# Performance work log

Hardware: AMD Instinct MI355X
Metric: run time of the kernel (lower is better)

The kernel has to match this reference:

```python
import jax, jax.numpy as jnp
import numpy as np

B, L, DIM, H = 2, 2048, 1024, 16
HD = DIM // H  # head dim = 64
MASK_SCALE = -10 * 6  # faithful to the original source: mask_expand *= -10 * 6


def setup_inputs() -> dict:
    key = jax.random.key(0)
    ks = jax.random.split(key, 8)
    s = 1.0 / np.sqrt(DIM)
    return {
        "x": jax.random.normal(ks[0], (B, L, DIM), jnp.float32),
        "attention_mask": jax.random.uniform(ks[1], (B, L, L), jnp.float32),
        "Wq": jax.random.normal(ks[2], (DIM, DIM), jnp.float32) * s,
        "bq": jnp.zeros((DIM,), jnp.float32),
        "Wk": jax.random.normal(ks[3], (DIM, DIM), jnp.float32) * s,
        "bk": jnp.zeros((DIM,), jnp.float32),
        "Wv": jax.random.normal(ks[4], (DIM, DIM), jnp.float32) * s,
        "bv": jnp.zeros((DIM,), jnp.float32),
    }


def _split_heads(t):
    # [B, L, DIM] -> [B, H, L, HD]
    return t.reshape(B, L, H, HD).transpose(0, 2, 1, 3)


def reference(x, attention_mask, Wq, bq, Wk, bk, Wv, bv):
    q = _split_heads(x @ Wq + bq)
    k = _split_heads(x @ Wk + bk)
    v = _split_heads(x @ Wv + bv)
    scale = float(HD) ** -0.5
    # full [B, H, L, L] score matrix, as in the original
    scores = jnp.einsum("bhqd,bhkd->bhqk", q, k) * scale
    scores = scores + attention_mask[:, None, :, :] * MASK_SCALE
    probs = jax.nn.softmax(scores, axis=-1)
    ctx = jnp.einsum("bhqk,bhkd->bhqd", probs, v)
    # merge heads back: [B, L, DIM]
    return ctx.transpose(0, 2, 1, 3).reshape(B, L, DIM)
```

## Files before the change

### kernel.cpp

```cpp
#include <hip/hip_runtime.h>

#define LL 2048
#define NHEADS 16
#define HDIM 64
#define QSCALE 0.18033688011112042f
#define MASKC1 -86.56170245333780f

typedef __attribute__((ext_vector_type(8))) __bf16 bf16x8;
typedef __attribute__((ext_vector_type(4))) float f32x4;

__device__ __forceinline__ unsigned short f2bf(float f) {
  unsigned int u = __builtin_bit_cast(unsigned int, f);
  u += 0x7fffu + ((u >> 16) & 1u);
  return (unsigned short)(u >> 16);
}

__device__ __forceinline__ bf16x8 ld_frag(const unsigned short* p) {
  return *reinterpret_cast<const bf16x8*>(p);
}

__device__ __forceinline__ void async_cp16(const unsigned short* g, unsigned short* l) {
  __builtin_amdgcn_global_load_lds(
      (const __attribute__((address_space(1))) unsigned int*)(unsigned long long)(g),
      (__attribute__((address_space(3))) unsigned int*)(unsigned int)(unsigned long long)(l),
      16, 0, 0);
}

__global__ __launch_bounds__(256) void cvt_x_kernel(const float* __restrict__ x,
                                                    unsigned short* __restrict__ xb) {
  int i = (blockIdx.x * 256 + threadIdx.x) * 4;
  float4 v = *reinterpret_cast<const float4*>(x + i);
  ushort4 o;
  o.x = f2bf(v.x); o.y = f2bf(v.y); o.z = f2bf(v.z); o.w = f2bf(v.w);
  *reinterpret_cast<ushort4*>(xb + i) = o;
}

__global__ __launch_bounds__(256) void transpose_w_kernel(const float* __restrict__ Wq,
                                                          const float* __restrict__ Wk,
                                                          const float* __restrict__ Wv,
                                                          unsigned short* __restrict__ WtAll) {
  int z = blockIdx.z;
  const float* W = (z == 0) ? Wq : (z == 1) ? Wk : Wv;
  unsigned short* dst = WtAll + (size_t)z * 1024 * 1024;
  int n0 = blockIdx.x * 64, k0 = blockIdx.y * 64;
  __shared__ float t[64][65];
  int tx = threadIdx.x & 63, ty = threadIdx.x >> 6;
#pragma unroll
  for (int p = 0; p < 16; ++p) {
    int kr = p * 4 + ty;
    t[kr][tx] = W[(size_t)(k0 + kr) * 1024 + n0 + tx];
  }
  __syncthreads();
#pragma unroll
  for (int p = 0; p < 16; ++p) {
    int nr = p * 4 + ty;
    dst[(size_t)(n0 + nr) * 1024 + k0 + tx] = f2bf(t[tx][nr]);
  }
}

__global__ __launch_bounds__(256) void em_prep_kernel(const float* __restrict__ mask,
                                                      unsigned short* __restrict__ em) {
  int row = blockIdx.y;
  int t = blockIdx.x * 256 + threadIdx.x;
  int kb = t >> 4, c = t & 15;
  const float* src = mask + (size_t)row * LL + kb * 64 + c;
  ushort4 o;
  o.x = f2bf(__builtin_amdgcn_exp2f(src[0]  * MASKC1));
  o.y = f2bf(__builtin_amdgcn_exp2f(src[16] * MASKC1));
  o.z = f2bf(__builtin_amdgcn_exp2f(src[32] * MASKC1));
  o.w = f2bf(__builtin_amdgcn_exp2f(src[48] * MASKC1));
  *reinterpret_cast<ushort4*>(em + (size_t)row * LL + kb * 64 + 4 * c) = o;
}

__global__ __launch_bounds__(256) void qkv_gemm_kernel(
    const unsigned short* __restrict__ xb, const unsigned short* __restrict__ WtAll,
    const float* __restrict__ bq, const float* __restrict__ bk, const float* __restrict__ bv,
    unsigned short* __restrict__ qkv) {
  const int z = blockIdx.z;
  const unsigned short* Wt = WtAll + (size_t)z * 1024 * 1024;
  const float* bias = (z == 0) ? bq : (z == 1) ? bk : bv;
  unsigned short* outb = qkv + (size_t)z * 4194304;

  __shared__ __align__(16) unsigned short smem[16384];
  unsigned short* As = smem;
  unsigned short* Bs = smem + 8192;

  const int tid = threadIdx.x;
  const int w = tid >> 6, lane = tid & 63, g = lane >> 4, cc = lane & 15;
  const int wm = w >> 1, wn = w & 1;
  const int m0 = blockIdx.y * 128, n0 = blockIdx.x * 128;
  const int srow = lane >> 3;
  const int gc = ((lane & 7) - srow) & 7;
  const unsigned short* ga = xb + (size_t)(m0 + w * 32 + srow) * 1024 + gc * 8;
  const unsigned short* gb = Wt + (size_t)(n0 + w * 32 + srow) * 1024 + gc * 8;
  unsigned short* la = As + w * 2048;
  unsigned short* lb = Bs + w * 2048;

  f32x4 acc[4][4];
#pragma unroll
  for (int i = 0; i < 4; ++i)
#pragma unroll
    for (int j = 0; j < 4; ++j) acc[i][j] = (f32x4)0.0f;

  for (int kk = 0; kk < 1024; kk += 64) {
    __syncthreads();
#pragma unroll
    for (int i = 0; i < 4; ++i) {
      async_cp16(ga + i * 8192 + kk, la + i * 512);
      async_cp16(gb + i * 8192 + kk, lb + i * 512);
    }
    __syncthreads();
    bf16x8 af[4][2], bfr[4][2];
#pragma unroll
    for (int mt = 0; mt < 4; ++mt)
#pragma unroll
      for (int ks = 0; ks < 2; ++ks)
        af[mt][ks] = ld_frag(&As[(wm * 64 + mt * 16 + cc) * 64 + ((4 * ks + g + cc) & 7) * 8]);
#pragma unroll
    for (int nt = 0; nt < 4; ++nt)
#pragma unroll
      for (int ks = 0; ks < 2; ++ks)
        bfr[nt][ks] = ld_frag(&Bs[(wn * 64 + nt * 16 + cc) * 64 + ((4 * ks + g + cc) & 7) * 8]);
#pragma unroll
    for (int mt = 0; mt < 4; ++mt)
#pragma unroll
      for (int nt = 0; nt < 4; ++nt)
#pragma unroll
        for (int ks = 0; ks < 2; ++ks)
          acc[mt][nt] = __builtin_amdgcn_mfma_f32_16x16x32_bf16(af[mt][ks], bfr[nt][ks],
                                                                acc[mt][nt], 0, 0, 0);
  }

  if (z != 2) {
    const float sc = (z == 0) ? QSCALE : 1.0f;
#pragma unroll
    for (int nt = 0; nt < 4; ++nt) {
      int n = n0 + wn * 64 + nt * 16 + cc;
      float bval = bias[n];
      int h = n >> 6, d = n & 63;
#pragma unroll
      for (int mt = 0; mt < 4; ++mt) {
#pragma unroll
        for (int r = 0; r < 4; ++r) {
          int m = m0 + wm * 64 + mt * 16 + g * 4 + r;
          int b = m >> 11, l = m & 2047;
          outb[(((size_t)(b * NHEADS + h) * LL) + l) * HDIM + d] =
              f2bf((acc[mt][nt][r] + bval) * sc);
        }
      }
    }
  } else {
    __syncthreads();
#pragma unroll
    for (int nt = 0; nt < 4; ++nt) {
      int nr = wn * 64 + nt * 16 + cc;
      float bval = bias[n0 + nr];
#pragma unroll
      for (int mt = 0; mt < 4; ++mt)
#pragma unroll
        for (int r = 0; r < 4; ++r)
          smem[nr * 128 + wm * 64 + 16 * g + 4 * r + mt] = f2bf(acc[mt][nt][r] + bval);
    }
    __syncthreads();
    int row = tid >> 1, half = tid & 1;
    int n = n0 + row, hh = n >> 6, dd = n & 63;
    int bb = m0 >> 11, l0 = (m0 & 2047) + half * 64;
    unsigned short* dst = outb + ((size_t)(bb * NHEADS + hh) * HDIM + dd) * LL + l0;
#pragma unroll
    for (int i = 0; i < 8; ++i)
      *reinterpret_cast<uint4*>(dst + i * 8) =
          *reinterpret_cast<const uint4*>(&smem[row * 128 + half * 64 + i * 8]);
  }
}

__global__ __launch_bounds__(256) void flash_kernel(
    const unsigned short* __restrict__ Qb, const unsigned short* __restrict__ Kb,
    const unsigned short* __restrict__ Vt, const unsigned short* __restrict__ Em,
    float* __restrict__ out) {
  const int bh = blockIdx.y, b = bh >> 4, h = bh & 15;
  const int q0 = blockIdx.x * 128;
  const int tid = threadIdx.x, w = tid >> 6, lane = tid & 63, g = lane >> 4, cc = lane & 15;
  const size_t bhoff = (size_t)bh * LL * HDIM;

  __shared__ __align__(16) unsigned short Ps[128 * 72];
  __shared__ __align__(16) unsigned short Ks[2][64 * 64];
  __shared__ __align__(16) unsigned short Vs[2][64 * 64];

  bf16x8 aq[2][2];
#pragma unroll
  for (int mt = 0; mt < 2; ++mt)
#pragma unroll
    for (int ks = 0; ks < 2; ++ks)
      aq[mt][ks] = *reinterpret_cast<const bf16x8*>(
          Qb + bhoff + (size_t)(q0 + w * 32 + mt * 16 + cc) * HDIM + ks * 32 + g * 8);

  const int srow = lane >> 3;
  const int gcs = ((lane & 7) - srow) & 7;
  const unsigned short* kg0 = Kb + bhoff + (size_t)(w * 8 + srow) * HDIM + gcs * 8;
  const unsigned short* kg1 = Kb + bhoff + (size_t)(32 + w * 8 + srow) * HDIM + gcs * 8;
  const unsigned short* vg0 = Vt + bhoff + (size_t)(w * 8 + srow) * LL + gcs * 8;
  const unsigned short* vg1 = Vt + bhoff + (size_t)(32 + w * 8 + srow) * LL + gcs * 8;

  float li[2][4];
  f32x4 oacc[2][4];
#pragma unroll
  for (int mt = 0; mt < 2; ++mt) {
#pragma unroll
    for (int r = 0; r < 4; ++r) li[mt][r] = 0.0f;
#pragma unroll
    for (int nt = 0; nt < 4; ++nt) oacc[mt][nt] = (f32x4)0.0f;
  }

  const unsigned short* embase = Em + ((size_t)b * LL + q0 + w * 32) * LL + 4 * cc;

  {
    async_cp16(kg0, Ks[0] + w * 512);
    async_cp16(kg1, Ks[0] + (w + 4) * 512);
    async_cp16(vg0, Vs[0] + w * 512);
    async_cp16(vg1, Vs[0] + (w + 4) * 512);
  }

  for (int kt = 0; kt < 32; ++kt) {
    const int buf = kt & 1;
    __syncthreads();
    if (kt + 1 < 32) {
      const int nb = buf ^ 1;
      async_cp16(kg0 + (size_t)(kt + 1) * 64 * HDIM, Ks[nb] + w * 512);
      async_cp16(kg1 + (size_t)(kt + 1) * 64 * HDIM, Ks[nb] + (w + 4) * 512);
      async_cp16(vg0 + (kt + 1) * 64, Vs[nb] + w * 512);
      async_cp16(vg1 + (kt + 1) * 64, Vs[nb] + (w + 4) * 512);
    }
    uint2 emv[2][4];
#pragma unroll
    for (int mt = 0; mt < 2; ++mt)
#pragma unroll
      for (int r = 0; r < 4; ++r)
        emv[mt][r] = *reinterpret_cast<const uint2*>(
            embase + (size_t)(mt * 16 + g * 4 + r) * LL + kt * 64);

    bf16x8 bk_[4][2];
#pragma unroll
    for (int nt = 0; nt < 4; ++nt)
#pragma unroll
      for (int ks = 0; ks < 2; ++ks)
        bk_[nt][ks] =
            ld_frag(&Ks[buf][(nt * 16 + cc) * 64 + ((4 * ks + g + cc) & 7) * 8]);
    f32x4 sacc[2][4];
#pragma unroll
    for (int mt = 0; mt < 2; ++mt)
#pragma unroll
      for (int nt = 0; nt < 4; ++nt) sacc[mt][nt] = (f32x4)0.0f;
#pragma unroll
    for (int mt = 0; mt < 2; ++mt)
#pragma unroll
      for (int nt = 0; nt < 4; ++nt)
#pragma unroll
        for (int ks = 0; ks < 2; ++ks)
          sacc[mt][nt] = __builtin_amdgcn_mfma_f32_16x16x32_bf16(aq[mt][ks], bk_[nt][ks],
                                                                 sacc[mt][nt], 0, 0, 0);

#pragma unroll
    for (int mt = 0; mt < 2; ++mt) {
#pragma unroll
      for (int r = 0; r < 4; ++r) {
        unsigned int ex = emv[mt][r].x, ey = emv[mt][r].y;
        float e0 = __builtin_bit_cast(float, ex << 16);
        float e1 = __builtin_bit_cast(float, ex & 0xffff0000u);
        float e2 = __builtin_bit_cast(float, ey << 16);
        float e3 = __builtin_bit_cast(float, ey & 0xffff0000u);
        float p0 = __builtin_amdgcn_exp2f(sacc[mt][0][r]) * e0;
        float p1 = __builtin_amdgcn_exp2f(sacc[mt][1][r]) * e1;
        float p2 = __builtin_amdgcn_exp2f(sacc[mt][2][r]) * e2;
        float p3 = __builtin_amdgcn_exp2f(sacc[mt][3][r]) * e3;
        unsigned int u01 = __builtin_amdgcn_perm(__builtin_bit_cast(unsigned int, p1),
                                                 __builtin_bit_cast(unsigned int, p0),
                                                 0x07060302u);
        unsigned int u23 = __builtin_amdgcn_perm(__builtin_bit_cast(unsigned int, p3),
                                                 __builtin_bit_cast(unsigned int, p2),
                                                 0x07060302u);
        li[mt][r] += __builtin_bit_cast(float, u01 << 16) +
                     __builtin_bit_cast(float, u01 & 0xffff0000u) +
                     __builtin_bit_cast(float, u23 << 16) +
                     __builtin_bit_cast(float, u23 & 0xffff0000u);
        uint2 pk; pk.x = u01; pk.y = u23;
        *reinterpret_cast<uint2*>(&Ps[(w * 32 + mt * 16 + g * 4 + r) * 72 + 4 * cc]) = pk;
      }
    }
    asm volatile("" ::: "memory");

    bf16x8 ap[2][2], bv[4][2];
#pragma unroll
    for (int mt = 0; mt < 2; ++mt)
#pragma unroll
      for (int ks = 0; ks < 2; ++ks)
        ap[mt][ks] = ld_frag(&Ps[(w * 32 + mt * 16 + cc) * 72 + ks * 32 + g * 8]);
#pragma unroll
    for (int nt = 0; nt < 4; ++nt)
#pragma unroll
      for (int ks = 0; ks < 2; ++ks)
        bv[nt][ks] =
            ld_frag(&Vs[buf][(nt * 16 + cc) * 64 + ((4 * ks + g + cc) & 7) * 8]);
#pragma unroll
    for (int mt = 0; mt < 2; ++mt)
#pragma unroll
      for (int nt = 0; nt < 4; ++nt)
#pragma unroll
        for (int ks = 0; ks < 2; ++ks)
          oacc[mt][nt] = __builtin_amdgcn_mfma_f32_16x16x32_bf16(ap[mt][ks], bv[nt][ks],
                                                                 oacc[mt][nt], 0, 0, 0);
  }

#pragma unroll
  for (int mt = 0; mt < 2; ++mt)
#pragma unroll
    for (int r = 0; r < 4; ++r) {
      float s = li[mt][r];
      s += __shfl_xor(s, 1);
      s += __shfl_xor(s, 2);
      s += __shfl_xor(s, 4);
      s += __shfl_xor(s, 8);
      float inv = 1.0f / s;
      int qrow = q0 + w * 32 + mt * 16 + g * 4 + r;
#pragma unroll
      for (int nt = 0; nt < 4; ++nt)
        out[((size_t)b * LL + qrow) * 1024 + h * 64 + nt * 16 + cc] = oacc[mt][nt][r] * inv;
    }
}

extern "C" void kernel_launch(void* const* d_in, const int* in_sizes, int n_in,
                              void* d_out, int out_size, void* d_ws, size_t ws_size,
                              hipStream_t stream) {
  const float* x    = (const float*)d_in[0];
  const float* mask = (const float*)d_in[1];
  const float* Wq   = (const float*)d_in[2];
  const float* bq   = (const float*)d_in[3];
  const float* Wk   = (const float*)d_in[4];
  const float* bk   = (const float*)d_in[5];
  const float* Wv   = (const float*)d_in[6];
  const float* bv   = (const float*)d_in[7];
  float* out = (float*)d_out;
  (void)in_sizes; (void)n_in; (void)out_size; (void)ws_size;

  char* ws = (char*)d_ws;
  unsigned short* qkv = (unsigned short*)(ws);
  unsigned short* xb  = (unsigned short*)(ws + (24u << 20));
  unsigned short* Wt  = (unsigned short*)(ws + (32u << 20));
  unsigned short* em  = (unsigned short*)(ws + (24u << 20));

  cvt_x_kernel<<<dim3(4096), dim3(256), 0, stream>>>(x, xb);
  transpose_w_kernel<<<dim3(16, 16, 3), dim3(256), 0, stream>>>(Wq, Wk, Wv, Wt);
  qkv_gemm_kernel<<<dim3(8, 32, 3), dim3(256), 0, stream>>>(xb, Wt, bq, bk, bv, qkv);
  em_prep_kernel<<<dim3(2, 4096), dim3(256), 0, stream>>>(mask, em);
  flash_kernel<<<dim3(16, 32), dim3(256), 0, stream>>>(qkv, qkv + 4194304, qkv + 8388608,
                                                       em, out);
}
```

Measured before the change: 214.9 us.

## Halve flash query tile to 64 rows, swizzle P buffer, merge prep kernels

The flash kernel now gives each block 64 query rows instead of 128, so each wave handles 16 rows. This doubles the grid to 1024 blocks and cuts registers and LDS per block, with launch bounds asking for 4 blocks per CU to raise occupancy. The P staging buffer switches from padded rows to an XOR-style swizzled 64-wide layout to avoid bank conflicts. The x conversion and weight transpose kernels are merged into one launch to save launch overhead. In exchange, K/V tiles are reloaded twice as often per query, and the loop is unrolled by 2.

```diff
diff --git a/kernel.cpp b/kernel.cpp
--- a/kernel.cpp
+++ b/kernel.cpp
@@ -26,35 +26,36 @@
       16, 0, 0);
 }
 
-__global__ __launch_bounds__(256) void cvt_x_kernel(const float* __restrict__ x,
-                                                    unsigned short* __restrict__ xb) {
-  int i = (blockIdx.x * 256 + threadIdx.x) * 4;
-  float4 v = *reinterpret_cast<const float4*>(x + i);
-  ushort4 o;
-  o.x = f2bf(v.x); o.y = f2bf(v.y); o.z = f2bf(v.z); o.w = f2bf(v.w);
-  *reinterpret_cast<ushort4*>(xb + i) = o;
-}
-
-__global__ __launch_bounds__(256) void transpose_w_kernel(const float* __restrict__ Wq,
-                                                          const float* __restrict__ Wk,
-                                                          const float* __restrict__ Wv,
-                                                          unsigned short* __restrict__ WtAll) {
-  int z = blockIdx.z;
-  const float* W = (z == 0) ? Wq : (z == 1) ? Wk : Wv;
-  unsigned short* dst = WtAll + (size_t)z * 1024 * 1024;
-  int n0 = blockIdx.x * 64, k0 = blockIdx.y * 64;
+__global__ __launch_bounds__(256) void prep_kernel(
+    const float* __restrict__ x, const float* __restrict__ Wq, const float* __restrict__ Wk,
+    const float* __restrict__ Wv, unsigned short* __restrict__ xb,
+    unsigned short* __restrict__ WtAll) {
   __shared__ float t[64][65];
-  int tx = threadIdx.x & 63, ty = threadIdx.x >> 6;
-#pragma unroll
-  for (int p = 0; p < 16; ++p) {
-    int kr = p * 4 + ty;
-    t[kr][tx] = W[(size_t)(k0 + kr) * 1024 + n0 + tx];
-  }
-  __syncthreads();
-#pragma unroll
-  for (int p = 0; p < 16; ++p) {
-    int nr = p * 4 + ty;
-    dst[(size_t)(n0 + nr) * 1024 + k0 + tx] = f2bf(t[tx][nr]);
+  int blk = blockIdx.x;
+  if (blk < 4096) {
+    int i = (blk * 256 + threadIdx.x) * 4;
+    float4 v = *reinterpret_cast<const float4*>(x + i);
+    ushort4 o;
+    o.x = f2bf(v.x); o.y = f2bf(v.y); o.z = f2bf(v.z); o.w = f2bf(v.w);
+    *reinterpret_cast<ushort4*>(xb + i) = o;
+  } else {
+    int idx = blk - 4096;
+    int z = idx >> 8; idx &= 255;
+    const float* W = (z == 0) ? Wq : (z == 1) ? Wk : Wv;
+    unsigned short* dst = WtAll + (size_t)z * 1024 * 1024;
+    int n0 = (idx & 15) * 64, k0 = (idx >> 4) * 64;
+    int tx = threadIdx.x & 63, ty = threadIdx.x >> 6;
+#pragma unroll
+    for (int p = 0; p < 16; ++p) {
+      int kr = p * 4 + ty;
+      t[kr][tx] = W[(size_t)(k0 + kr) * 1024 + n0 + tx];
+    }
+    __syncthreads();
+#pragma unroll
+    for (int p = 0; p < 16; ++p) {
+      int nr = p * 4 + ty;
+      dst[(size_t)(n0 + nr) * 1024 + k0 + tx] = f2bf(t[tx][nr]);
+    }
   }
 }
 
@@ -173,26 +174,24 @@
   }
 }
 
-__global__ __launch_bounds__(256) void flash_kernel(
+__global__ __launch_bounds__(256, 4) void flash_kernel(
     const unsigned short* __restrict__ Qb, const unsigned short* __restrict__ Kb,
     const unsigned short* __restrict__ Vt, const unsigned short* __restrict__ Em,
     float* __restrict__ out) {
   const int bh = blockIdx.y, b = bh >> 4, h = bh & 15;
-  const int q0 = blockIdx.x * 128;
+  const int q0 = blockIdx.x * 64;
   const int tid = threadIdx.x, w = tid >> 6, lane = tid & 63, g = lane >> 4, cc = lane & 15;
   const size_t bhoff = (size_t)bh * LL * HDIM;
 
-  __shared__ __align__(16) unsigned short Ps[128 * 72];
+  __shared__ __align__(16) unsigned short Ps[64 * 64];
   __shared__ __align__(16) unsigned short Ks[2][64 * 64];
   __shared__ __align__(16) unsigned short Vs[2][64 * 64];
 
-  bf16x8 aq[2][2];
-#pragma unroll
-  for (int mt = 0; mt < 2; ++mt)
-#pragma unroll
-    for (int ks = 0; ks < 2; ++ks)
-      aq[mt][ks] = *reinterpret_cast<const bf16x8*>(
-          Qb + bhoff + (size_t)(q0 + w * 32 + mt * 16 + cc) * HDIM + ks * 32 + g * 8);
+  bf16x8 aq[2];
+#pragma unroll
+  for (int ks = 0; ks < 2; ++ks)
+    aq[ks] = *reinterpret_cast<const bf16x8*>(
+        Qb + bhoff + (size_t)(q0 + w * 16 + cc) * HDIM + ks * 32 + g * 8);
 
   const int srow = lane >> 3;
   const int gcs = ((lane & 7) - srow) & 7;
@@ -201,25 +200,21 @@
   const unsigned short* vg0 = Vt + bhoff + (size_t)(w * 8 + srow) * LL + gcs * 8;
   const unsigned short* vg1 = Vt + bhoff + (size_t)(32 + w * 8 + srow) * LL + gcs * 8;
 
-  float li[2][4];
-  f32x4 oacc[2][4];
-#pragma unroll
-  for (int mt = 0; mt < 2; ++mt) {
-#pragma unroll
-    for (int r = 0; r < 4; ++r) li[mt][r] = 0.0f;
-#pragma unroll
-    for (int nt = 0; nt < 4; ++nt) oacc[mt][nt] = (f32x4)0.0f;
-  }
-
-  const unsigned short* embase = Em + ((size_t)b * LL + q0 + w * 32) * LL + 4 * cc;
-
-  {
-    async_cp16(kg0, Ks[0] + w * 512);
-    async_cp16(kg1, Ks[0] + (w + 4) * 512);
-    async_cp16(vg0, Vs[0] + w * 512);
-    async_cp16(vg1, Vs[0] + (w + 4) * 512);
-  }
-
+  float li[4];
+  f32x4 oacc[4];
+#pragma unroll
+  for (int r = 0; r < 4; ++r) li[r] = 0.0f;
+#pragma unroll
+  for (int nt = 0; nt < 4; ++nt) oacc[nt] = (f32x4)0.0f;
+
+  const unsigned short* embase = Em + ((size_t)b * LL + q0 + w * 16) * LL + 4 * cc;
+
+  async_cp16(kg0, Ks[0] + w * 512);
+  async_cp16(kg1, Ks[0] + (w + 4) * 512);
+  async_cp16(vg0, Vs[0] + w * 512);
+  async_cp16(vg1, Vs[0] + (w + 4) * 512);
+
+#pragma unroll 2
   for (int kt = 0; kt < 32; ++kt) {
     const int buf = kt & 1;
     __syncthreads();
@@ -230,101 +225,86 @@
       async_cp16(vg0 + (kt + 1) * 64, Vs[nb] + w * 512);
       async_cp16(vg1 + (kt + 1) * 64, Vs[nb] + (w + 4) * 512);
     }
-    uint2 emv[2][4];
-#pragma unroll
-    for (int mt = 0; mt < 2; ++mt)
-#pragma unroll
-      for (int r = 0; r < 4; ++r)
-        emv[mt][r] = *reinterpret_cast<const uint2*>(
-            embase + (size_t)(mt * 16 + g * 4 + r) * LL + kt * 64);
+    uint2 emv[4];
+#pragma unroll
+    for (int r = 0; r < 4; ++r)
+      emv[r] = *reinterpret_cast<const uint2*>(embase + (size_t)(g * 4 + r) * LL + kt * 64);
 
     bf16x8 bk_[4][2];
 #pragma unroll
     for (int nt = 0; nt < 4; ++nt)
 #pragma unroll
       for (int ks = 0; ks < 2; ++ks)
-        bk_[nt][ks] =
-            ld_frag(&Ks[buf][(nt * 16 + cc) * 64 + ((4 * ks + g + cc) & 7) * 8]);
-    f32x4 sacc[2][4];
-#pragma unroll
-    for (int mt = 0; mt < 2; ++mt)
-#pragma unroll
-      for (int nt = 0; nt < 4; ++nt) sacc[mt][nt] = (f32x4)0.0f;
-#pragma unroll
-    for (int mt = 0; mt < 2; ++mt)
-#pragma unroll
-      for (int nt = 0; nt < 4; ++nt)
-#pragma unroll
-        for (int ks = 0; ks < 2; ++ks)
-          sacc[mt][nt] = __builtin_amdgcn_mfma_f32_16x16x32_bf16(aq[mt][ks], bk_[nt][ks],
-                                                                 sacc[mt][nt], 0, 0, 0);
-
-#pragma unroll
-    for (int mt = 0; mt < 2; ++mt) {
-#pragma unroll
-      for (int r = 0; r < 4; ++r) {
-        unsigned int ex = emv[mt][r].x, ey = emv[mt][r].y;
-        float e0 = __builtin_bit_cast(float, ex << 16);
-        float e1 = __builtin_bit_cast(float, ex & 0xffff0000u);
-        float e2 = __builtin_bit_cast(float, ey << 16);
-        float e3 = __builtin_bit_cast(float, ey & 0xffff0000u);
-        float p0 = __builtin_amdgcn_exp2f(sacc[mt][0][r]) * e0;
-        float p1 = __builtin_amdgcn_exp2f(sacc[mt][1][r]) * e1;
-        float p2 = __builtin_amdgcn_exp2f(sacc[mt][2][r]) * e2;
-        float p3 = __builtin_amdgcn_exp2f(sacc[mt][3][r]) * e3;
-        unsigned int u01 = __builtin_amdgcn_perm(__builtin_bit_cast(unsigned int, p1),
-                                                 __builtin_bit_cast(unsigned int, p0),
-                                                 0x07060302u);
-        unsigned int u23 = __builtin_amdgcn_perm(__builtin_bit_cast(unsigned int, p3),
-                                                 __builtin_bit_cast(unsigned int, p2),
-                                                 0x07060302u);
-        li[mt][r] += __builtin_bit_cast(float, u01 << 16) +
-                     __builtin_bit_cast(float, u01 & 0xffff0000u) +
-                     __builtin_bit_cast(float, u23 << 16) +
-                     __builtin_bit_cast(float, u23 & 0xffff0000u);
-        uint2 pk; pk.x = u01; pk.y = u23;
-        *reinterpret_cast<uint2*>(&Ps[(w * 32 + mt * 16 + g * 4 + r) * 72 + 4 * cc]) = pk;
-      }
+        bk_[nt][ks] = ld_frag(&Ks[buf][(nt * 16 + cc) * 64 + ((4 * ks + g + cc) & 7) * 8]);
+    f32x4 sacc[4];
+#pragma unroll
+    for (int nt = 0; nt < 4; ++nt) sacc[nt] = (f32x4)0.0f;
+#pragma unroll
+    for (int nt = 0; nt < 4; ++nt)
+#pragma unroll
+      for (int ks = 0; ks < 2; ++ks)
+        sacc[nt] = __builtin_amdgcn_mfma_f32_16x16x32_bf16(aq[ks], bk_[nt][ks], sacc[nt], 0, 0, 0);
+
+#pragma unroll
+    for (int r = 0; r < 4; ++r) {
+      unsigned int ex = emv[r].x, ey = emv[r].y;
+      float e0 = __builtin_bit_cast(float, ex << 16);
+      float e1 = __builtin_bit_cast(float, ex & 0xffff0000u);
+      float e2 = __builtin_bit_cast(float, ey << 16);
+      float e3 = __builtin_bit_cast(float, ey & 0xffff0000u);
+      float p0 = __builtin_amdgcn_exp2f(sacc[0][r]) * e0;
+      float p1 = __builtin_amdgcn_exp2f(sacc[1][r]) * e1;
+      float p2 = __builtin_amdgcn_exp2f(sacc[2][r]) * e2;
+      float p3 = __builtin_amdgcn_exp2f(sacc[3][r]) * e3;
+      unsigned int u01 = __builtin_amdgcn_perm(__builtin_bit_cast(unsigned int, p1),
+                                               __builtin_bit_cast(unsigned int, p0),
+                                               0x07060302u);
+      unsigned int u23 = __builtin_amdgcn_perm(__builtin_bit_cast(unsigned int, p3),
+                                               __builtin_bit_cast(unsigned int, p2),
+                                               0x07060302u);
+      li[r] += __builtin_bit_cast(float, u01 << 16) +
+               __builtin_bit_cast(float, u01 & 0xffff0000u) +
+               __builtin_bit_cast(float, u23 << 16) +
+               __builtin_bit_cast(float, u23 & 0xffff0000u);
+      uint2 pk; pk.x = u01; pk.y = u23;
+      int prow = w * 16 + g * 4 + r;
+      int poff = prow * 64 + ((((cc >> 1) + prow) & 7) << 3) + ((cc & 1) << 2);
+      *reinterpret_cast<uint2*>(&Ps[poff]) = pk;
     }
     asm volatile("" ::: "memory");
 
-    bf16x8 ap[2][2], bv[4][2];
-#pragma unroll
-    for (int mt = 0; mt < 2; ++mt)
-#pragma unroll
-      for (int ks = 0; ks < 2; ++ks)
-        ap[mt][ks] = ld_frag(&Ps[(w * 32 + mt * 16 + cc) * 72 + ks * 32 + g * 8]);
-#pragma unroll
-    for (int nt = 0; nt < 4; ++nt)
-#pragma unroll
-      for (int ks = 0; ks < 2; ++ks)
-        bv[nt][ks] =
-            ld_frag(&Vs[buf][(nt * 16 + cc) * 64 + ((4 * ks + g + cc) & 7) * 8]);
-#pragma unroll
-    for (int mt = 0; mt < 2; ++mt)
-#pragma unroll
-      for (int nt = 0; nt < 4; ++nt)
-#pragma unroll
-        for (int ks = 0; ks < 2; ++ks)
-          oacc[mt][nt] = __builtin_amdgcn_mfma_f32_16x16x32_bf16(ap[mt][ks], bv[nt][ks],
-                                                                 oacc[mt][nt], 0, 0, 0);
-  }
-
-#pragma unroll
-  for (int mt = 0; mt < 2; ++mt)
-#pragma unroll
-    for (int r = 0; r < 4; ++r) {
-      float s = li[mt][r];
-      s += __shfl_xor(s, 1);
-      s += __shfl_xor(s, 2);
-      s += __shfl_xor(s, 4);
-      s += __shfl_xor(s, 8);
-      float inv = 1.0f / s;
-      int qrow = q0 + w * 32 + mt * 16 + g * 4 + r;
-#pragma unroll
-      for (int nt = 0; nt < 4; ++nt)
-        out[((size_t)b * LL + qrow) * 1024 + h * 64 + nt * 16 + cc] = oacc[mt][nt][r] * inv;
-    }
+    bf16x8 ap[2], bv[4][2];
+    {
+      int arow = w * 16 + cc;
+#pragma unroll
+      for (int ks = 0; ks < 2; ++ks)
+        ap[ks] = ld_frag(&Ps[arow * 64 + (((ks * 4 + g + arow) & 7) << 3)]);
+    }
+#pragma unroll
+    for (int nt = 0; nt < 4; ++nt)
+#pragma unroll
+      for (int ks = 0; ks < 2; ++ks)
+        bv[nt][ks] = ld_frag(&Vs[buf][(nt * 16 + cc) * 64 + ((4 * ks + g + cc) & 7) * 8]);
+#pragma unroll
+    for (int nt = 0; nt < 4; ++nt)
+#pragma unroll
+      for (int ks = 0; ks < 2; ++ks)
+        oacc[nt] = __builtin_amdgcn_mfma_f32_16x16x32_bf16(ap[ks], bv[nt][ks], oacc[nt], 0, 0, 0);
+  }
+
+#pragma unroll
+  for (int r = 0; r < 4; ++r) {
+    float s = li[r];
+    s += __shfl_xor(s, 1);
+    s += __shfl_xor(s, 2);
+    s += __shfl_xor(s, 4);
+    s += __shfl_xor(s, 8);
+    float inv = 1.0f / s;
+    int qrow = q0 + w * 16 + g * 4 + r;
+#pragma unroll
+    for (int nt = 0; nt < 4; ++nt)
+      out[((size_t)b * LL + qrow) * 1024 + h * 64 + nt * 16 + cc] = oacc[nt][r] * inv;
+  }
 }
 
 extern "C" void kernel_launch(void* const* d_in, const int* in_sizes, int n_in,
@@ -347,10 +327,9 @@
   unsigned short* Wt  = (unsigned short*)(ws + (32u << 20));
   unsigned short* em  = (unsigned short*)(ws + (24u << 20));
 
-  cvt_x_kernel<<<dim3(4096), dim3(256), 0, stream>>>(x, xb);
-  transpose_w_kernel<<<dim3(16, 16, 3), dim3(256), 0, stream>>>(Wq, Wk, Wv, Wt);
+  prep_kernel<<<dim3(4864), dim3(256), 0, stream>>>(x, Wq, Wk, Wv, xb, Wt);
   qkv_gemm_kernel<<<dim3(8, 32, 3), dim3(256), 0, stream>>>(xb, Wt, bq, bk, bv, qkv);
   em_prep_kernel<<<dim3(2, 4096), dim3(256), 0, stream>>>(mask, em);
-  flash_kernel<<<dim3(16, 32), dim3(256), 0, stream>>>(qkv, qkv + 4194304, qkv + 8388608,
+  flash_kernel<<<dim3(32, 32), dim3(256), 0, stream>>>(qkv, qkv + 4194304, qkv + 8388608,
                                                        em, out);
 }
```

After: 214.9 us. No clear change (+0.0%).
